# Performance work log

Hardware: AMD Instinct MI355X
Metric: run time of the kernel (lower is better)

## Reference

```python
import jax, jax.numpy as jnp
import numpy as np

B, D, K = 8192, 512, 4096
MAX_WORD_LENGTH = 16
RESIDUAL_THRESHOLD = 0.01
DECAY_FACTOR = 0.95
EPS_TARGET = 1e-8


def setup_inputs() -> dict:
    key = jax.random.key(0)
    k1, k2 = jax.random.split(key)
    targets = jax.random.normal(k1, (B, D), dtype=jnp.float32)
    codebook = jax.random.normal(k2, (K, D), dtype=jnp.float32)
    return {"targets": targets, "codebook": codebook}


def reference(targets, codebook):
    """Batched greedy residual pursuit (allow_negative_signs=True).

    Returns:
      seq      [B, L] int32 signed indices (>=0: add idx; <0: subtract (-idx-1)); 0 where inactive
      mask     [B, L] bool, True where a step actually emitted a symbol
      residual [B, D] final residual after pursuit
    """
    target_norm = jnp.linalg.norm(targets, axis=-1)  # [B]

    def step(residual, step_idx):
        rnorm = jnp.linalg.norm(residual, axis=-1)  # [B]
        active = (rnorm >= RESIDUAL_THRESHOLD) & (target_norm >= EPS_TARGET)
        # cosine similarity of each codebook vector with residual direction
        res_dir = residual / jnp.maximum(rnorm, 1e-12)[:, None]
        cos = jnp.einsum('bd,kd->bk', res_dir, codebook)  # [B, K]
        best = jnp.argmax(jnp.abs(cos), axis=-1)  # [B]
        best_cos = jnp.take_along_axis(cos, best[:, None], axis=-1)[:, 0]
        signed = jnp.where(best_cos >= 0, best, -(best + 1)).astype(jnp.int32)
        sign = jnp.where(best_cos >= 0, 1.0, -1.0).astype(residual.dtype)
        decay = jnp.power(jnp.asarray(DECAY_FACTOR, residual.dtype),
                          (step_idx + 1).astype(residual.dtype))
        contrib = sign[:, None] * decay * codebook[best]  # [B, D]
        new_res = jnp.where(active[:, None], residual - contrib, residual)
        out_idx = jnp.where(active, signed, 0)
        return new_res, (out_idx, active)

    residual, (seq, mask) = jax.lax.scan(step, targets, jnp.arange(MAX_WORD_LENGTH))
    return seq.T, mask.T, residual
```

## Files before the change

### kernel.cpp

```cpp
#include <hip/hip_runtime.h>
#include <hip/hip_bf16.h>

#define B_SZ 8192
#define D_SZ 512
#define K_SZ 4096
#define L_SZ 16
#define M_ALL (B_SZ + K_SZ)

typedef __attribute__((ext_vector_type(8))) short short8v;
typedef __attribute__((ext_vector_type(4))) float f32x4;
typedef _Float16 half8v __attribute__((ext_vector_type(8)));

__global__ void cast_bf16_kernel(const float* __restrict__ targets,
                                 const float* __restrict__ codebook,
                                 __hip_bfloat16* __restrict__ abf) {
    int idx = blockIdx.x * blockDim.x + threadIdx.x;
    const int total4 = (M_ALL * D_SZ) / 4;
    if (idx >= total4) return;
    int base = idx * 4;
    const float* src = (base < B_SZ * D_SZ) ? (targets + base)
                                            : (codebook + (base - B_SZ * D_SZ));
    float4 v = *(const float4*)src;
    abf[base + 0] = __float2bfloat16(v.x);
    abf[base + 1] = __float2bfloat16(v.y);
    abf[base + 2] = __float2bfloat16(v.z);
    abf[base + 3] = __float2bfloat16(v.w);
}

__global__ void cn2_kernel(const float* __restrict__ codebook,
                           double* __restrict__ cn2) {
    int row  = blockIdx.x * 4 + (threadIdx.x >> 6);
    int lane = threadIdx.x & 63;
    const float* r = codebook + (size_t)row * D_SZ;
    double s = 0.0;
#pragma unroll
    for (int j = 0; j < 8; j++) { double v = (double)r[lane + 64 * j]; s += v * v; }
#pragma unroll
    for (int o = 32; o > 0; o >>= 1) s += __shfl_down(s, o, 64);
    if (lane == 0) cn2[row] = s;
}

#define BM 128
#define BN 128
#define BK 32
#define LDSS 40

__global__ __launch_bounds__(256, 2)
void gemm_bt_kernel(const __hip_bfloat16* __restrict__ A,
                    const __hip_bfloat16* __restrict__ Bm,
                    _Float16* __restrict__ C) {
    __shared__ short As[BM * LDSS];
    __shared__ short Bs[BN * LDSS];
    const int tid  = threadIdx.x;
    const int bm   = blockIdx.y * BM;
    const int bn   = blockIdx.x * BN;
    const int wave = tid >> 6, lane = tid & 63;
    const int wm = (wave & 1) * 64, wn = (wave >> 1) * 64;
    const int row16 = lane & 15, quad = lane >> 4;
    const int koff = quad * 8;

    f32x4 acc[4][4] = {};

    const int srow = tid >> 1;
    const int scol = (tid & 1) * 16;
    const short* Ag = (const short*)A;
    const short* Bg = (const short*)Bm;

    for (int k0 = 0; k0 < D_SZ; k0 += BK) {
        short8v a0 = *(const short8v*)(Ag + (size_t)(bm + srow) * D_SZ + k0 + scol);
        short8v a1 = *(const short8v*)(Ag + (size_t)(bm + srow) * D_SZ + k0 + scol + 8);
        short8v b0 = *(const short8v*)(Bg + (size_t)(bn + srow) * D_SZ + k0 + scol);
        short8v b1 = *(const short8v*)(Bg + (size_t)(bn + srow) * D_SZ + k0 + scol + 8);
        __syncthreads();
        *(short8v*)(As + srow * LDSS + scol)     = a0;
        *(short8v*)(As + srow * LDSS + scol + 8) = a1;
        *(short8v*)(Bs + srow * LDSS + scol)     = b0;
        *(short8v*)(Bs + srow * LDSS + scol + 8) = b1;
        __syncthreads();

        short8v af[4], bf[4];
#pragma unroll
        for (int i = 0; i < 4; i++)
            af[i] = *(const short8v*)(As + (wm + i * 16 + row16) * LDSS + koff);
#pragma unroll
        for (int j = 0; j < 4; j++)
            bf[j] = *(const short8v*)(Bs + (wn + j * 16 + row16) * LDSS + koff);
#pragma unroll
        for (int i = 0; i < 4; i++)
#pragma unroll
            for (int j = 0; j < 4; j++)
                acc[i][j] = __builtin_amdgcn_mfma_f32_16x16x32_bf16(af[i], bf[j], acc[i][j], 0, 0, 0);
    }

#pragma unroll
    for (int i = 0; i < 4; i++) {
        int grow = bm + wm + i * 16 + quad * 4;
#pragma unroll
        for (int j = 0; j < 4; j++) {
            int gcol = bn + wn + j * 16 + row16;
#pragma unroll
            for (int r = 0; r < 4; r++)
                C[(size_t)(grow + r) * K_SZ + gcol] = (_Float16)acc[i][j][r];
        }
    }
}

#define MAXC 64
#define MARGIN 2.0f

__global__ __launch_bounds__(256, 4)
void pursuit_kernel(const float* __restrict__ targets,
                    const float* __restrict__ codebook,
                    const _Float16* __restrict__ S,
                    const double* __restrict__ cn2,
                    float* __restrict__ out) {
    const int b = blockIdx.x;
    const int tid = threadIdx.x;
    const int lane = tid & 63, wave = tid >> 6;

    __shared__ double rres[D_SZ];
    __shared__ double redD[4];
    __shared__ float  redF[4];
    __shared__ int    cand_k[MAXC];
    __shared__ double cand_v[MAXC];
    __shared__ int    ncand;
    __shared__ int    s_best;
    __shared__ double s_sd;
    __shared__ double s_rn2;

    float g_r[16];
    {
        const _Float16* g0 = S + (size_t)b * K_SZ;
#pragma unroll
        for (int j = 0; j < 2; j++) {
            half8v h = *(const half8v*)(g0 + j * 2048 + 8 * tid);
#pragma unroll
            for (int e = 0; e < 8; e++) g_r[8 * j + e] = (float)h[e];
        }
    }

    double loc = 0.0;
#pragma unroll
    for (int j = 0; j < 2; j++) {
        int i = tid + 256 * j;
        double v = (double)targets[(size_t)b * D_SZ + i];
        rres[i] = v;
        loc += v * v;
    }
#pragma unroll
    for (int o = 32; o > 0; o >>= 1) loc += __shfl_down(loc, o, 64);
    if (lane == 0) redD[wave] = loc;
    __syncthreads();
    const double tn2 = redD[0] + redD[1] + redD[2] + redD[3];
    if (tid == 0) s_rn2 = tn2;
    __syncthreads();
    const bool tgt_ok = (sqrt(tn2) >= 1e-8);

    float* out_seq  = out;
    float* out_mask = out + (size_t)B_SZ * L_SZ;
    float* out_res  = out + (size_t)2 * B_SZ * L_SZ;

    double decay = 1.0;
    for (int t = 0; t < L_SZ; t++) {
        decay *= 0.95;
        double rn2 = s_rn2;
        bool active = (sqrt(rn2) >= 0.01) && tgt_ok;
        if (!active) {
            if (tid == 0) {
                out_seq[(size_t)b * L_SZ + t]  = 0.0f;
                out_mask[(size_t)b * L_SZ + t] = 0.0f;
            }
            continue;
        }

        float m = 0.0f;
#pragma unroll
        for (int j = 0; j < 16; j++) m = fmaxf(m, fabsf(g_r[j]));
#pragma unroll
        for (int o = 32; o > 0; o >>= 1) m = fmaxf(m, __shfl_down(m, o, 64));
        if (lane == 0) redF[wave] = m;
        if (tid == 0) ncand = 0;
        __syncthreads();
        float M = fmaxf(fmaxf(redF[0], redF[1]), fmaxf(redF[2], redF[3]));
        float thr = M - MARGIN;

#pragma unroll
        for (int j = 0; j < 2; j++)
#pragma unroll
            for (int e = 0; e < 8; e++) {
                if (fabsf(g_r[8 * j + e]) >= thr) {
                    int p = atomicAdd(&ncand, 1);
                    if (p < MAXC) cand_k[p] = j * 2048 + 8 * tid + e;
                }
            }
        __syncthreads();
        int nc = min(ncand, MAXC);

        for (int ci = wave; ci < nc; ci += 4) {
            int k = cand_k[ci];
            const float* crow = codebook + (size_t)k * D_SZ;
            double sum = 0.0;
#pragma unroll
            for (int j = 0; j < 8; j++)
                sum += rres[lane + 64 * j] * (double)crow[lane + 64 * j];
#pragma unroll
            for (int o = 32; o > 0; o >>= 1) sum += __shfl_down(sum, o, 64);
            if (lane == 0) cand_v[ci] = sum;
        }
        __syncthreads();

        if (tid == 0) {
            int bk = cand_k[0]; double bv = cand_v[0];
            for (int c = 1; c < nc; c++) {
                int k2 = cand_k[c]; double v2 = cand_v[c];
                if (fabs(v2) > fabs(bv) || (fabs(v2) == fabs(bv) && k2 < bk)) { bk = k2; bv = v2; }
            }
            double sd = ((bv >= 0.0) ? 1.0 : -1.0) * decay;
            s_best = bk;
            s_sd = sd;
            s_rn2 = rn2 - 2.0 * sd * bv + sd * sd * cn2[bk];
            out_seq[(size_t)b * L_SZ + t]  = (float)((bv >= 0.0) ? bk : (-bk - 1));
            out_mask[(size_t)b * L_SZ + t] = 1.0f;
        }
        __syncthreads();
        const int bk = s_best;
        const double sd = s_sd;
        const float sdf = (float)sd;

        const _Float16* Grow = S + (size_t)(B_SZ + bk) * K_SZ;
#pragma unroll
        for (int j = 0; j < 2; j++) {
            half8v h = *(const half8v*)(Grow + j * 2048 + 8 * tid);
#pragma unroll
            for (int e = 0; e < 8; e++) g_r[8 * j + e] -= sdf * (float)h[e];
        }
        const float* crow = codebook + (size_t)bk * D_SZ;
#pragma unroll
        for (int j = 0; j < 2; j++) {
            int i = tid + 256 * j;
            rres[i] = rres[i] - sd * (double)crow[i];
        }
    }

#pragma unroll
    for (int j = 0; j < 2; j++) {
        int i = tid + 256 * j;
        out_res[(size_t)b * D_SZ + i] = (float)rres[i];
    }
}

extern "C" void kernel_launch(void* const* d_in, const int* in_sizes, int n_in,
                              void* d_out, int out_size, void* d_ws, size_t ws_size,
                              hipStream_t stream) {
    const float* targets  = (const float*)d_in[0];
    const float* codebook = (const float*)d_in[1];
    float* out = (float*)d_out;

    __hip_bfloat16* abf = (__hip_bfloat16*)d_ws;
    _Float16* S = (_Float16*)((char*)d_ws + (size_t)M_ALL * D_SZ * 2);
    double* cn2 = (double*)((char*)d_ws + (size_t)M_ALL * D_SZ * 2
                                        + (size_t)M_ALL * K_SZ * 2);

    int total4 = (M_ALL * D_SZ) / 4;
    cast_bf16_kernel<<<(total4 + 255) / 256, 256, 0, stream>>>(targets, codebook, abf);
    cn2_kernel<<<K_SZ / 4, 256, 0, stream>>>(codebook, cn2);

    dim3 ggrid(K_SZ / BN, M_ALL / BM);
    gemm_bt_kernel<<<ggrid, 256, 0, stream>>>(abf, abf + (size_t)B_SZ * D_SZ, S);

    pursuit_kernel<<<B_SZ, 256, 0, stream>>>(targets, codebook, S, cn2, out);
}
```

Before: 396.4 us.

## Map one wave per batch row in pursuit kernel, removing block barriers

The pursuit kernel now handles one batch row per 64-lane wave instead of one per 256-thread block. Each lane keeps 64 Gram entries and 8 residual doubles in registers. All per-step reductions use wave shuffles, which removes the shared-memory staging and the several __syncthreads per step. Candidate margin and cap are also reduced (MARGIN 2→1, MAXC 64→32), so fewer exact fp64 dot products are evaluated, at some risk of missing the true argmax given the fp16/bf16 Gram error. Register pressure rises sharply with 64 floats plus 8 doubles per lane under launch_bounds(256,4).

```diff
diff --git a/kernel.cpp b/kernel.cpp
--- a/kernel.cpp
+++ b/kernel.cpp
@@ -105,8 +105,8 @@
     }
 }
 
-#define MAXC 64
-#define MARGIN 2.0f
+#define MAXC 32
+#define MARGIN 1.0f
 
 __global__ __launch_bounds__(256, 4)
 void pursuit_kernel(const float* __restrict__ targets,
@@ -114,46 +114,42 @@
                     const _Float16* __restrict__ S,
                     const double* __restrict__ cn2,
                     float* __restrict__ out) {
-    const int b = blockIdx.x;
-    const int tid = threadIdx.x;
-    const int lane = tid & 63, wave = tid >> 6;
-
-    __shared__ double rres[D_SZ];
-    __shared__ double redD[4];
-    __shared__ float  redF[4];
-    __shared__ int    cand_k[MAXC];
-    __shared__ double cand_v[MAXC];
-    __shared__ int    ncand;
-    __shared__ int    s_best;
-    __shared__ double s_sd;
-    __shared__ double s_rn2;
-
-    float g_r[16];
+    const int wave = threadIdx.x >> 6;
+    const int lane = threadIdx.x & 63;
+    const int b = blockIdx.x * 4 + wave;
+    const int lane8 = lane * 8;
+
+    __shared__ int s_cnt[4];
+    __shared__ int s_cand[4][MAXC];
+    int* cnt  = &s_cnt[wave];
+    int* cand = s_cand[wave];
+
+    float g_r[64];
     {
-        const _Float16* g0 = S + (size_t)b * K_SZ;
-#pragma unroll
-        for (int j = 0; j < 2; j++) {
-            half8v h = *(const half8v*)(g0 + j * 2048 + 8 * tid);
-#pragma unroll
-            for (int e = 0; e < 8; e++) g_r[8 * j + e] = (float)h[e];
-        }
-    }
-
+        const _Float16* g0 = S + (size_t)b * K_SZ + lane8;
+#pragma unroll
+        for (int jb = 0; jb < 8; jb++) {
+            half8v h = *(const half8v*)(g0 + jb * 512);
+#pragma unroll
+            for (int e = 0; e < 8; e++) g_r[jb * 8 + e] = (float)h[e];
+        }
+    }
+
+    double rres[8];
     double loc = 0.0;
-#pragma unroll
-    for (int j = 0; j < 2; j++) {
-        int i = tid + 256 * j;
-        double v = (double)targets[(size_t)b * D_SZ + i];
-        rres[i] = v;
-        loc += v * v;
-    }
-#pragma unroll
-    for (int o = 32; o > 0; o >>= 1) loc += __shfl_down(loc, o, 64);
-    if (lane == 0) redD[wave] = loc;
-    __syncthreads();
-    const double tn2 = redD[0] + redD[1] + redD[2] + redD[3];
-    if (tid == 0) s_rn2 = tn2;
-    __syncthreads();
+    {
+        const float* tg = targets + (size_t)b * D_SZ + lane8;
+        float4 t0 = *(const float4*)tg;
+        float4 t1 = *(const float4*)(tg + 4);
+        rres[0] = t0.x; rres[1] = t0.y; rres[2] = t0.z; rres[3] = t0.w;
+        rres[4] = t1.x; rres[5] = t1.y; rres[6] = t1.z; rres[7] = t1.w;
+#pragma unroll
+        for (int e = 0; e < 8; e++) loc += rres[e] * rres[e];
+    }
+#pragma unroll
+    for (int o = 32; o > 0; o >>= 1) loc += __shfl_xor(loc, o, 64);
+    const double tn2 = loc;
+    double rn2 = tn2;
     const bool tgt_ok = (sqrt(tn2) >= 1e-8);
 
     float* out_seq  = out;
@@ -163,10 +159,9 @@
     double decay = 1.0;
     for (int t = 0; t < L_SZ; t++) {
         decay *= 0.95;
-        double rn2 = s_rn2;
         bool active = (sqrt(rn2) >= 0.01) && tgt_ok;
         if (!active) {
-            if (tid == 0) {
+            if (lane == 0) {
                 out_seq[(size_t)b * L_SZ + t]  = 0.0f;
                 out_mask[(size_t)b * L_SZ + t] = 0.0f;
             }
@@ -175,77 +170,75 @@
 
         float m = 0.0f;
 #pragma unroll
-        for (int j = 0; j < 16; j++) m = fmaxf(m, fabsf(g_r[j]));
-#pragma unroll
-        for (int o = 32; o > 0; o >>= 1) m = fmaxf(m, __shfl_down(m, o, 64));
-        if (lane == 0) redF[wave] = m;
-        if (tid == 0) ncand = 0;
-        __syncthreads();
-        float M = fmaxf(fmaxf(redF[0], redF[1]), fmaxf(redF[2], redF[3]));
+        for (int j = 0; j < 64; j++) m = fmaxf(m, fabsf(g_r[j]));
+        float M = m;
+#pragma unroll
+        for (int o = 32; o > 0; o >>= 1) M = fmaxf(M, __shfl_xor(M, o, 64));
         float thr = M - MARGIN;
 
-#pragma unroll
-        for (int j = 0; j < 2; j++)
-#pragma unroll
-            for (int e = 0; e < 8; e++) {
-                if (fabsf(g_r[8 * j + e]) >= thr) {
-                    int p = atomicAdd(&ncand, 1);
-                    if (p < MAXC) cand_k[p] = j * 2048 + 8 * tid + e;
-                }
-            }
-        __syncthreads();
-        int nc = min(ncand, MAXC);
-
-        for (int ci = wave; ci < nc; ci += 4) {
-            int k = cand_k[ci];
-            const float* crow = codebook + (size_t)k * D_SZ;
-            double sum = 0.0;
-#pragma unroll
-            for (int j = 0; j < 8; j++)
-                sum += rres[lane + 64 * j] * (double)crow[lane + 64 * j];
-#pragma unroll
-            for (int o = 32; o > 0; o >>= 1) sum += __shfl_down(sum, o, 64);
-            if (lane == 0) cand_v[ci] = sum;
-        }
-        __syncthreads();
-
-        if (tid == 0) {
-            int bk = cand_k[0]; double bv = cand_v[0];
-            for (int c = 1; c < nc; c++) {
-                int k2 = cand_k[c]; double v2 = cand_v[c];
-                if (fabs(v2) > fabs(bv) || (fabs(v2) == fabs(bv) && k2 < bk)) { bk = k2; bv = v2; }
-            }
-            double sd = ((bv >= 0.0) ? 1.0 : -1.0) * decay;
-            s_best = bk;
-            s_sd = sd;
-            s_rn2 = rn2 - 2.0 * sd * bv + sd * sd * cn2[bk];
+        if (lane == 0) *cnt = 0;
+        if (m >= thr) {
+#pragma unroll
+            for (int jb = 0; jb < 8; jb++)
+#pragma unroll
+                for (int e = 0; e < 8; e++)
+                    if (fabsf(g_r[jb * 8 + e]) >= thr) {
+                        int p = atomicAdd(cnt, 1);
+                        if (p < MAXC) cand[p] = jb * 512 + lane8 + e;
+                    }
+        }
+        __threadfence_block();
+        int nc = min(*cnt, MAXC);
+
+        int bk = -1; double bv = 0.0; bool have = false;
+        for (int ci = 0; ci < nc; ci++) {
+            int k = cand[ci];
+            const float* crow = codebook + (size_t)k * D_SZ + lane8;
+            float4 c0 = *(const float4*)crow;
+            float4 c1 = *(const float4*)(crow + 4);
+            double s = rres[0] * (double)c0.x + rres[1] * (double)c0.y
+                     + rres[2] * (double)c0.z + rres[3] * (double)c0.w
+                     + rres[4] * (double)c1.x + rres[5] * (double)c1.y
+                     + rres[6] * (double)c1.z + rres[7] * (double)c1.w;
+#pragma unroll
+            for (int o = 32; o > 0; o >>= 1) s += __shfl_xor(s, o, 64);
+            if (!have || fabs(s) > fabs(bv) ||
+                (fabs(s) == fabs(bv) && k < bk)) { bk = k; bv = s; have = true; }
+        }
+
+        double sd = ((bv >= 0.0) ? 1.0 : -1.0) * decay;
+        rn2 = rn2 - 2.0 * sd * bv + sd * sd * cn2[bk];
+        if (lane == 0) {
             out_seq[(size_t)b * L_SZ + t]  = (float)((bv >= 0.0) ? bk : (-bk - 1));
             out_mask[(size_t)b * L_SZ + t] = 1.0f;
         }
-        __syncthreads();
-        const int bk = s_best;
-        const double sd = s_sd;
         const float sdf = (float)sd;
 
-        const _Float16* Grow = S + (size_t)(B_SZ + bk) * K_SZ;
-#pragma unroll
-        for (int j = 0; j < 2; j++) {
-            half8v h = *(const half8v*)(Grow + j * 2048 + 8 * tid);
-#pragma unroll
-            for (int e = 0; e < 8; e++) g_r[8 * j + e] -= sdf * (float)h[e];
-        }
-        const float* crow = codebook + (size_t)bk * D_SZ;
-#pragma unroll
-        for (int j = 0; j < 2; j++) {
-            int i = tid + 256 * j;
-            rres[i] = rres[i] - sd * (double)crow[i];
-        }
-    }
-
-#pragma unroll
-    for (int j = 0; j < 2; j++) {
-        int i = tid + 256 * j;
-        out_res[(size_t)b * D_SZ + i] = (float)rres[i];
+        const _Float16* Grow = S + (size_t)(B_SZ + bk) * K_SZ + lane8;
+#pragma unroll
+        for (int jb = 0; jb < 8; jb++) {
+            half8v h = *(const half8v*)(Grow + jb * 512);
+#pragma unroll
+            for (int e = 0; e < 8; e++) g_r[jb * 8 + e] -= sdf * (float)h[e];
+        }
+        const float* crow = codebook + (size_t)bk * D_SZ + lane8;
+        {
+            float4 c0 = *(const float4*)crow;
+            float4 c1 = *(const float4*)(crow + 4);
+            rres[0] -= sd * (double)c0.x; rres[1] -= sd * (double)c0.y;
+            rres[2] -= sd * (double)c0.z; rres[3] -= sd * (double)c0.w;
+            rres[4] -= sd * (double)c1.x; rres[5] -= sd * (double)c1.y;
+            rres[6] -= sd * (double)c1.z; rres[7] -= sd * (double)c1.w;
+        }
+    }
+
+    {
+        float* o = out_res + (size_t)b * D_SZ + lane8;
+        float4 r0, r1;
+        r0.x = (float)rres[0]; r0.y = (float)rres[1]; r0.z = (float)rres[2]; r0.w = (float)rres[3];
+        r1.x = (float)rres[4]; r1.y = (float)rres[5]; r1.z = (float)rres[6]; r1.w = (float)rres[7];
+        *(float4*)o = r0;
+        *(float4*)(o + 4) = r1;
     }
 }
 
@@ -268,5 +261,5 @@
     dim3 ggrid(K_SZ / BN, M_ALL / BM);
     gemm_bt_kernel<<<ggrid, 256, 0, stream>>>(abf, abf + (size_t)B_SZ * D_SZ, S);
 
-    pursuit_kernel<<<B_SZ, 256, 0, stream>>>(targets, codebook, S, cn2, out);
-}
+    pursuit_kernel<<<B_SZ / 4, 256, 0, stream>>>(targets, codebook, S, cn2, out);
+}
```

Measured after the change: 382.8 us. 3.4% less time.
